# Performance work log

Hardware: AMD Instinct MI355X
Metric: run time of the kernel (lower is better)

## Reference

```python
import jax, jax.numpy as jnp
import numpy as np
import math

FACTOR = 5

def setup_inputs() -> dict:
    key = jax.random.key(0)
    k1, k2, k3, k4 = jax.random.split(key, 4)
    B, L, H, D = 8, 4096, 8, 64
    sample_k = FACTOR * int(np.ceil(np.log(L)))  # 45
    return {
        "queries": jax.random.normal(k1, (B, L, H, D), dtype=jnp.float32),
        "keys": jax.random.normal(k2, (B, L, H, D), dtype=jnp.float32),
        "values": jax.random.normal(k3, (B, L, H, D), dtype=jnp.float32),
        "index_sample": jax.random.randint(k4, (L, sample_k), 0, L, dtype=jnp.int64),
    }


def reference(queries, keys, values, index_sample):
    B, L_Q, H, D = queries.shape
    L_K = keys.shape[1]
    # [B, H, L, D]
    Q = jnp.transpose(queries, (0, 2, 1, 3))
    K = jnp.transpose(keys, (0, 2, 1, 3))
    V = jnpp = jnp.transpose(values, (0, 2, 1, 3))

    u = min(FACTOR * int(math.ceil(math.log(L_Q))), L_Q)  # n_top

    # --- _prob_QK ---
    # sampled keys: [B, H, L_Q, sample_k, D]
    K_sample = K[:, :, index_sample, :]
    # Q_K_sample: [B, H, L_Q, sample_k]
    Q_K_sample = jnp.einsum("bhqd,bhqsd->bhqs", Q, K_sample)
    M = jnp.max(Q_K_sample, axis=-1) - jnp.sum(Q_K_sample, axis=-1) / L_K
    _, M_top = jax.lax.top_k(M, u)  # [B, H, u]
    Q_reduce = jnp.take_along_axis(Q, M_top[..., None], axis=2)  # [B, H, u, D]
    scores = jnp.einsum("bhud,bhkd->bhuk", Q_reduce, K)  # [B, H, u, L_K]

    scale = 1.0 / math.sqrt(D)
    scores = scores * scale

    # --- initial context (mask_flag=True): causal cumsum of V ---
    context = jnp.cumsum(V, axis=2)  # [B, H, L_V, D]

    # --- causal ProbMask: key position j invalid if j > query position ---
    key_pos = jnp.arange(L_K)
    mask = key_pos[None, None, None, :] > M_top[..., None]  # [B, H, u, L_K]
    scores = jnp.where(mask, -jnp.inf, scores)

    attn = jax.nn.softmax(scores, axis=-1)  # dropout is identity at eval
    values_agg = jnp.einsum("bhuk,bhkd->bhud", attn, V)  # [B, H, u, D]

    b_idx = jnp.arange(B)[:, None, None]
    h_idx = jnp.arange(H)[None, :, None]
    context = context.at[b_idx, h_idx, M_top].set(values_agg)

    return jnp.transpose(context, (0, 2, 1, 3))  # [B, L_Q, H, D]
```

## Files before the change

kernel.cpp:

```cpp
#include <hip/hip_runtime.h>
#include <math.h>

#define Bc 8
#define Lc 4096
#define Hc 8
#define Dc 64
#define CHUNK 512
#define NCH (Lc / CHUNK)
#define VCH 16
#define VROWS (Lc / VCH)

template<int CTRL>
__device__ __forceinline__ float dpp_radd(float v) {
    int y = __builtin_amdgcn_update_dpp(0, __float_as_int(v), CTRL, 0xF, 0xF, true);
    return v + __int_as_float(y);
}
__device__ __forceinline__ float row16_sum(float p) {
    p = dpp_radd<0x128>(p);
    p = dpp_radd<0x124>(p);
    p = dpp_radd<0x122>(p);
    p = dpp_radd<0x121>(p);
    return p;
}

template<int S>
__global__ __launch_bounds__(256) void k_meas_t(
    const float* __restrict__ Q, const float* __restrict__ K,
    const int* __restrict__ idx, float* __restrict__ M)
{
    constexpr int NIT = (S + 3) / 4;
    int b = blockIdx.z, h = blockIdx.y;
    int w = threadIdx.x >> 6, lane = threadIdx.x & 63;
    int q = blockIdx.x * 4 + w;
    int grp = lane >> 4, gl = lane & 15;

    const float4 qv = *(const float4*)(Q + (((size_t)b * Lc + q) * Hc + h) * Dc + gl * 4);
    const int* ip = idx + (size_t)q * S + grp;
    const float* Kb = K + ((size_t)b * Lc * Hc + h) * Dc + gl * 4;

    int rows[NIT];
    #pragma unroll
    for (int it = 0; it < NIT - 1; it++) rows[it] = ip[it * 4];
    {
        int s = 4 * (NIT - 1) + grp;
        rows[NIT - 1] = ip[(s < S) ? 4 * (NIT - 1) : (S - 1 - grp)];
    }

    float mloc = -INFINITY, sloc = 0.f;
    #pragma unroll
    for (int it = 0; it < NIT; it++) {
        const float4 kw = *(const float4*)(Kb + ((size_t)rows[it] << 9));
        float p = kw.x * qv.x + kw.y * qv.y + kw.z * qv.z + kw.w * qv.w;
        p = row16_sum(p);
        int s = it * 4 + grp;
        if (s < S) { mloc = fmaxf(mloc, p); sloc += p; }
    }
    mloc = fmaxf(mloc, __shfl_xor(mloc, 16, 64));
    mloc = fmaxf(mloc, __shfl_xor(mloc, 32, 64));
    sloc += __shfl_xor(sloc, 16, 64);
    sloc += __shfl_xor(sloc, 32, 64);

    if (lane == 0)
        M[((size_t)(b * Hc + h)) * Lc + q] = mloc - sloc * (1.0f / (float)Lc);
}

__global__ __launch_bounds__(256) void k_meas_dyn(
    const float* __restrict__ Q, const float* __restrict__ K,
    const int* __restrict__ idx, float* __restrict__ M, int S)
{
    int b = blockIdx.z, h = blockIdx.y;
    int w = threadIdx.x >> 6, lane = threadIdx.x & 63;
    int q = blockIdx.x * 4 + w;
    int grp = lane >> 4, gl = lane & 15;

    const float4 qv = *(const float4*)(Q + (((size_t)b * Lc + q) * Hc + h) * Dc + gl * 4);
    const int* ip = idx + (size_t)q * S;
    const float* Kb = K + ((size_t)b * Lc * Hc + h) * Dc + gl * 4;

    float mloc = -INFINITY, sloc = 0.f;
    int niter = (S + 3) >> 2;
    for (int it = 0; it < niter; it++) {
        int s = it * 4 + grp;
        int ii = s < S ? s : S - 1;
        int row = ip[ii];
        const float4 kw = *(const float4*)(Kb + ((size_t)row << 9));
        float p = kw.x * qv.x + kw.y * qv.y + kw.z * qv.z + kw.w * qv.w;
        p = row16_sum(p);
        if (s < S) { mloc = fmaxf(mloc, p); sloc += p; }
    }
    mloc = fmaxf(mloc, __shfl_xor(mloc, 16, 64));
    mloc = fmaxf(mloc, __shfl_xor(mloc, 32, 64));
    sloc += __shfl_xor(sloc, 16, 64);
    sloc += __shfl_xor(sloc, 32, 64);
    if (lane == 0)
        M[((size_t)(b * Hc + h)) * Lc + q] = mloc - sloc * (1.0f / (float)Lc);
}

__global__ __launch_bounds__(256) void k_topk(
    const float* __restrict__ M, int* __restrict__ top, int U)
{
    int bh = blockIdx.x;
    int tid = threadIdx.x;
    const float* m = M + (size_t)bh * Lc;

    unsigned long long key[16];
    #pragma unroll
    for (int j = 0; j < 16; j++) {
        int i = tid * 16 + j;
        unsigned int u = __float_as_uint(m[i]);
        u ^= (unsigned int)(((int)u >> 31)) | 0x80000000u;
        key[j] = ((unsigned long long)u << 32) | (unsigned int)i;
    }
    unsigned long long myb = key[0];
    #pragma unroll
    for (int j = 1; j < 16; j++) myb = key[j] > myb ? key[j] : myb;

    __shared__ unsigned long long swave[2][4];

    for (int u = 0; u < U; u++) {
        unsigned long long wmax = myb;
        #pragma unroll
        for (int o = 32; o >= 1; o >>= 1) {
            unsigned long long t = __shfl_xor(wmax, o, 64);
            wmax = t > wmax ? t : wmax;
        }
        if ((tid & 63) == 0) swave[u & 1][tid >> 6] = wmax;
        __syncthreads();
        unsigned long long w0 = swave[u & 1][0], w1 = swave[u & 1][1];
        unsigned long long w2 = swave[u & 1][2], w3 = swave[u & 1][3];
        unsigned long long a = w0 > w1 ? w0 : w1;
        unsigned long long c = w2 > w3 ? w2 : w3;
        unsigned long long win = a > c ? a : c;
        int widx = (int)(win & 0xFFFFFFFFu);
        if (tid == 0) top[(size_t)bh * U + u] = widx;
        if (tid == (widx >> 4)) {
            #pragma unroll
            for (int j = 0; j < 16; j++) if (j == (widx & 15)) key[j] = 0ull;
            unsigned long long b2 = key[0];
            #pragma unroll
            for (int j = 1; j < 16; j++) b2 = key[j] > b2 ? key[j] : b2;
            myb = b2;
        }
    }
}

__global__ __launch_bounds__(256) void k_vsum(
    const float* __restrict__ V, float* __restrict__ bsum)
{
    int b = blockIdx.z, h = blockIdx.y, c = blockIdx.x;
    int d = threadIdx.x & 63, g = threadIdx.x >> 6;
    __shared__ float part[4][64];
    float s = 0.f;
    int r0 = c * VROWS;
    for (int r = r0 + g; r < r0 + VROWS; r += 4)
        s += V[(((size_t)b * Lc + r) * Hc + h) * Dc + d];
    part[g][d] = s;
    __syncthreads();
    if (g == 0)
        bsum[(((size_t)(b * Hc + h)) * VCH + c) * 64 + d] =
            part[0][d] + part[1][d] + part[2][d] + part[3][d];
}

__global__ __launch_bounds__(256) void k_scan(
    const float* __restrict__ V, const float* __restrict__ bsum,
    float* __restrict__ out)
{
    int b = blockIdx.z, h = blockIdx.y, c = blockIdx.x;
    int d = threadIdx.x & 63, g = threadIdx.x >> 6;
    int bh = b * Hc + h;
    __shared__ float gtot[4][64];
    __shared__ float goff[4][64];

    float base = 0.f;
    for (int cc = 0; cc < c; cc++)
        base += bsum[((size_t)bh * VCH + cc) * 64 + d];

    int gs = c * VROWS + g * 64;
    float gsum = 0.f;
    for (int r = gs; r < gs + 64; r++)
        gsum += V[(((size_t)b * Lc + r) * Hc + h) * Dc + d];
    gtot[g][d] = gsum;
    __syncthreads();
    if (g == 0) {
        float run = base;
        for (int gg = 0; gg < 4; gg++) { goff[gg][d] = run; run += gtot[gg][d]; }
    }
    __syncthreads();
    float run = goff[g][d];
    for (int r = gs; r < gs + 64; r++) {
        size_t o = (((size_t)b * Lc + r) * Hc + h) * Dc + d;
        run += V[o];
        out[o] = run;
    }
}

__global__ __launch_bounds__(256) void k_attn2(
    const float* __restrict__ Q, const float* __restrict__ K,
    const float* __restrict__ V, const int* __restrict__ top,
    float* __restrict__ Opart, float* __restrict__ Mp, float* __restrict__ Lp,
    int U)
{
    int b = blockIdx.z, h = blockIdx.y, c = blockIdx.x;
    int bh = b * Hc + h;
    int tid = threadIdx.x;
    int lane = tid & 63, g = tid >> 6;

    __shared__ float sQ[45][64];
    __shared__ int   sqi[45];
    __shared__ float sKT[64][65];
    __shared__ float sVT[64][65];
    __shared__ float sP[45][64];

    if (tid < U) sqi[tid] = top[(size_t)bh * U + tid];
    __syncthreads();
    for (int u = g; u < U; u += 4)
        sQ[u][lane] = Q[(((size_t)b * Lc + sqi[u]) * Hc + h) * Dc + lane] * 0.125f;

    int nj = 0, uj[12], qj[12];
    for (int u = g; u < U; u += 4) { uj[nj] = u; qj[nj] = sqi[u]; nj++; }

    float m_r[12], l_r[12], o_r[12];
    #pragma unroll
    for (int j = 0; j < 12; j++) { m_r[j] = -INFINITY; l_r[j] = 0.f; o_r[j] = 0.f; }

    int k0c = c * CHUNK;
    for (int t = 0; t < CHUNK / 64; t++) {
        int k0 = k0c + t * 64;
        __syncthreads();
        {
            const float* kp = K + (((size_t)b * Lc + k0 + lane) * Hc + h) * Dc + g * 16;
            const float* vp = V + (((size_t)b * Lc + k0 + lane) * Hc + h) * Dc + g * 16;
            #pragma unroll
            for (int i = 0; i < 4; i++) {
                float4 kw = *(const float4*)(kp + i * 4);
                float4 vw = *(const float4*)(vp + i * 4);
                int d0 = g * 16 + i * 4;
                sKT[d0+0][lane] = kw.x; sKT[d0+1][lane] = kw.y;
                sKT[d0+2][lane] = kw.z; sKT[d0+3][lane] = kw.w;
                sVT[d0+0][lane] = vw.x; sVT[d0+1][lane] = vw.y;
                sVT[d0+2][lane] = vw.z; sVT[d0+3][lane] = vw.w;
            }
        }
        __syncthreads();

        for (int j = 0; j < nj; j++) {
            int q = qj[j];
            if (k0 > q) continue;
            int u = uj[j];
            float s = 0.f;
            #pragma unroll
            for (int d = 0; d < 64; d += 4) {
                float k0v = sKT[d+0][lane];
                float k1v = sKT[d+1][lane];
                float k2v = sKT[d+2][lane];
                float k3v = sKT[d+3][lane];
                float4 qv = *(const float4*)&sQ[u][d];
                s += qv.x*k0v + qv.y*k1v + qv.z*k2v + qv.w*k3v;
            }
            if (k0 + lane > q) s = -INFINITY;
            float tm = s;
            #pragma unroll
            for (int o = 32; o >= 1; o >>= 1) tm = fmaxf(tm, __shfl_xor(tm, o, 64));
            float mnew = fmaxf(m_r[j], tm);
            float p = __expf(s - mnew);
            float ps = p;
            #pragma unroll
            for (int o = 32; o >= 1; o >>= 1) ps += __shfl_xor(ps, o, 64);
            float alpha = __expf(m_r[j] - mnew);
            l_r[j] = l_r[j] * alpha + ps;
            m_r[j] = mnew;
            sP[u][lane] = p;
            float pv = 0.f;
            #pragma unroll
            for (int k = 0; k < 64; k += 4) {
                float v0 = sVT[lane][k+0];
                float v1 = sVT[lane][k+1];
                float v2 = sVT[lane][k+2];
                float v3 = sVT[lane][k+3];
                float4 pw = *(const float4*)&sP[u][k];
                pv += pw.x*v0 + pw.y*v1 + pw.z*v2 + pw.w*v3;
            }
            o_r[j] = o_r[j] * alpha + pv;
        }
    }

    for (int j = 0; j < nj; j++) {
        int u = uj[j];
        size_t s0 = ((size_t)bh * NCH + c) * U + u;
        Opart[s0 * 64 + lane] = o_r[j];
        if (lane == 0) { Mp[s0] = m_r[j]; Lp[s0] = l_r[j]; }
    }
}

__global__ __launch_bounds__(64) void k_combine(
    const float* __restrict__ Opart, const float* __restrict__ Mp,
    const float* __restrict__ Lp, const int* __restrict__ top,
    float* __restrict__ out, int U)
{
    int b = blockIdx.z, h = blockIdx.y, u = blockIdx.x;
    int bh = b * Hc + h;
    int lane = threadIdx.x;
    int q = top[(size_t)bh * U + u];

    float mv[NCH], lv[NCH];
    float mg = -INFINITY;
    #pragma unroll
    for (int c = 0; c < NCH; c++) {
        size_t s0 = ((size_t)bh * NCH + c) * U + u;
        mv[c] = Mp[s0]; lv[c] = Lp[s0];
        mg = fmaxf(mg, mv[c]);
    }
    float Ls = 0.f, o = 0.f;
    #pragma unroll
    for (int c = 0; c < NCH; c++) {
        if (lv[c] > 0.f) {
            float w = __expf(mv[c] - mg);
            Ls += w * lv[c];
            o  += w * Opart[(((size_t)bh * NCH + c) * U + u) * 64 + lane];
        }
    }
    out[(((size_t)b * Lc + q) * Hc + h) * Dc + lane] = o / Ls;
}

extern "C" void kernel_launch(void* const* d_in, const int* in_sizes, int n_in,
                              void* d_out, int out_size, void* d_ws, size_t ws_size,
                              hipStream_t stream)
{
    const float* Q = (const float*)d_in[0];
    const float* K = (const float*)d_in[1];
    const float* V = (const float*)d_in[2];
    const int* idx = (const int*)d_in[3];
    float* out = (float*)d_out;

    int S = in_sizes[3] / Lc;

    char* ws = (char*)d_ws;
    float* M     = (float*)ws;
    float* Opart = (float*)ws;
    float* Mp    = (float*)(ws + 6291456);
    float* Lp    = (float*)(ws + 6422528);
    float* bsum  = (float*)(ws + 6815744);
    int*   top   = (int*)  (ws + 8388608);

    dim3 blk(256);
    if (S == 45)
        k_meas_t<45><<<dim3(Lc / 4, Hc, Bc), blk, 0, stream>>>(Q, K, idx, M);
    else
        k_meas_dyn  <<<dim3(Lc / 4, Hc, Bc), blk, 0, stream>>>(Q, K, idx, M, S);
    k_topk   <<<dim3(Bc * Hc),        blk, 0, stream>>>(M, top, S);
    k_vsum   <<<dim3(VCH, Hc, Bc),    blk, 0, stream>>>(V, bsum);
    k_scan   <<<dim3(VCH, Hc, Bc),    blk, 0, stream>>>(V, bsum, out);
    k_attn2  <<<dim3(NCH, Hc, Bc),    blk, 0, stream>>>(Q, K, V, top, Opart, Mp, Lp, S);
    k_combine<<<dim3(S, Hc, Bc), dim3(64), 0, stream>>>(Opart, Mp, Lp, top, out, S);
}
```

Before: 641.2 us.

## Batch four queries per K/V tile pass, sort queries, and balance causal chunks

Reworks the sparse-query attention kernel. Each wave now processes four top-u queries at once so every K and V value read from shared memory is reused four times. Per-wave query slots are bitonic-sorted by position so causally dead groups are skipped together. Chunk boundaries are non-uniform to balance causal work, tiles past the largest selected query are skipped, and K is stored in a swizzled float4 layout with DPP-based wave reductions. In exchange it uses more registers and duplicates padded slots, whose partial outputs are written redundantly.

```diff
diff --git a/kernel.cpp b/kernel.cpp
--- a/kernel.cpp
+++ b/kernel.cpp
@@ -5,22 +5,38 @@
 #define Lc 4096
 #define Hc 8
 #define Dc 64
-#define CHUNK 512
-#define NCH (Lc / CHUNK)
+#define NCH 8
 #define VCH 16
 #define VROWS (Lc / VCH)
 
+__constant__ int c_cb[NCH + 1] = {0, 256, 576, 832, 1216, 1600, 2048, 2624, 4096};
+
+template<int CTRL>
+__device__ __forceinline__ float dpp_mov(float v) {
+    return __int_as_float(__builtin_amdgcn_update_dpp(
+        0, __float_as_int(v), CTRL, 0xF, 0xF, true));
+}
 template<int CTRL>
 __device__ __forceinline__ float dpp_radd(float v) {
-    int y = __builtin_amdgcn_update_dpp(0, __float_as_int(v), CTRL, 0xF, 0xF, true);
-    return v + __int_as_float(y);
+    return v + dpp_mov<CTRL>(v);
 }
 __device__ __forceinline__ float row16_sum(float p) {
-    p = dpp_radd<0x128>(p);
-    p = dpp_radd<0x124>(p);
-    p = dpp_radd<0x122>(p);
-    p = dpp_radd<0x121>(p);
+    p = dpp_radd<0x128>(p); p = dpp_radd<0x124>(p);
+    p = dpp_radd<0x122>(p); p = dpp_radd<0x121>(p);
     return p;
+}
+__device__ __forceinline__ float wmax64(float v) {
+    v = fmaxf(v, dpp_mov<0x128>(v));
+    v = fmaxf(v, dpp_mov<0x124>(v));
+    v = fmaxf(v, dpp_mov<0x122>(v));
+    v = fmaxf(v, dpp_mov<0x121>(v));
+    v = fmaxf(v, __shfl_xor(v, 16, 64));
+    return fmaxf(v, __shfl_xor(v, 32, 64));
+}
+__device__ __forceinline__ float wsum64(float v) {
+    v = row16_sum(v);
+    v += __shfl_xor(v, 16, 64);
+    return v + __shfl_xor(v, 32, 64);
 }
 
 template<int S>
@@ -205,26 +221,62 @@
     int tid = threadIdx.x;
     int lane = tid & 63, g = tid >> 6;
 
-    __shared__ float sQ[45][64];
-    __shared__ int   sqi[45];
-    __shared__ float sKT[64][65];
-    __shared__ float sVT[64][65];
-    __shared__ float sP[45][64];
+    __shared__ float4 sK4[64][16];
+    __shared__ float  sVT[64][65];
+    __shared__ float  sQ[45][64];
+    __shared__ float  sP[45][64];
+    __shared__ int    sqi[45];
 
     if (tid < U) sqi[tid] = top[(size_t)bh * U + tid];
     __syncthreads();
     for (int u = g; u < U; u += 4)
         sQ[u][lane] = Q[(((size_t)b * Lc + sqi[u]) * Hc + h) * Dc + lane] * 0.125f;
 
-    int nj = 0, uj[12], qj[12];
-    for (int u = g; u < U; u += 4) { uj[nj] = u; qj[nj] = sqi[u]; nj++; }
+    int qbm = 0;
+    for (int u = 0; u < U; u++) qbm = max(qbm, sqi[u]);
+
+    int qq[16], tt[16];
+    int ulast = g + (((U - 1 - g) >> 2) << 2);
+    #pragma unroll
+    for (int i = 0; i < 12; i++) {
+        int u = g + 4 * i;
+        u = (u <= ulast) ? u : ulast;
+        tt[i] = u; qq[i] = sqi[u];
+    }
+    #pragma unroll
+    for (int i = 12; i < 16; i++) { tt[i] = tt[11]; qq[i] = 0x7FFFFFFF; }
+    #pragma unroll
+    for (int kk = 2; kk <= 16; kk <<= 1) {
+        #pragma unroll
+        for (int jj = kk >> 1; jj > 0; jj >>= 1) {
+            #pragma unroll
+            for (int ii = 0; ii < 16; ii++) {
+                int ll = ii ^ jj;
+                if (ll > ii) {
+                    bool up = ((ii & kk) == 0);
+                    bool sw = up ? (qq[ii] > qq[ll]) : (qq[ii] < qq[ll]);
+                    if (sw) {
+                        int tq = qq[ii]; qq[ii] = qq[ll]; qq[ll] = tq;
+                        int tu = tt[ii]; tt[ii] = tt[ll]; tt[ll] = tu;
+                    }
+                }
+            }
+        }
+    }
 
     float m_r[12], l_r[12], o_r[12];
     #pragma unroll
     for (int j = 0; j < 12; j++) { m_r[j] = -INFINITY; l_r[j] = 0.f; o_r[j] = 0.f; }
 
-    int k0c = c * CHUNK;
-    for (int t = 0; t < CHUNK / 64; t++) {
+    int k0c = c_cb[c], k1c = c_cb[c + 1];
+    int ntile = 0;
+    if (qbm >= k0c) {
+        int lastk = min(qbm, k1c - 1);
+        ntile = (lastk - k0c) / 64 + 1;
+    }
+    int kswz = lane & 7;
+
+    for (int t = 0; t < ntile; t++) {
         int k0 = k0c + t * 64;
         __syncthreads();
         {
@@ -234,58 +286,72 @@
             for (int i = 0; i < 4; i++) {
                 float4 kw = *(const float4*)(kp + i * 4);
                 float4 vw = *(const float4*)(vp + i * 4);
-                int d0 = g * 16 + i * 4;
-                sKT[d0+0][lane] = kw.x; sKT[d0+1][lane] = kw.y;
-                sKT[d0+2][lane] = kw.z; sKT[d0+3][lane] = kw.w;
+                int lb = g * 4 + i;
+                sK4[lane][lb ^ (lane & 7)] = kw;
+                int d0 = lb * 4;
                 sVT[d0+0][lane] = vw.x; sVT[d0+1][lane] = vw.y;
                 sVT[d0+2][lane] = vw.z; sVT[d0+3][lane] = vw.w;
             }
         }
         __syncthreads();
 
-        for (int j = 0; j < nj; j++) {
-            int q = qj[j];
-            if (k0 > q) continue;
-            int u = uj[j];
-            float s = 0.f;
-            #pragma unroll
-            for (int d = 0; d < 64; d += 4) {
-                float k0v = sKT[d+0][lane];
-                float k1v = sKT[d+1][lane];
-                float k2v = sKT[d+2][lane];
-                float k3v = sKT[d+3][lane];
-                float4 qv = *(const float4*)&sQ[u][d];
-                s += qv.x*k0v + qv.y*k1v + qv.z*k2v + qv.w*k3v;
+        #pragma unroll
+        for (int j0 = 0; j0 < 12; j0 += 4) {
+            if (k0 > qq[j0 + 3]) continue;
+            int ua = tt[j0], ub = tt[j0+1], uc = tt[j0+2], ud = tt[j0+3];
+            float s0 = 0.f, s1 = 0.f, s2 = 0.f, s3 = 0.f;
+            #pragma unroll
+            for (int lb = 0; lb < 16; lb++) {
+                float4 kb = sK4[lane][lb ^ kswz];
+                float4 qa = *(const float4*)&sQ[ua][lb * 4];
+                float4 qb = *(const float4*)&sQ[ub][lb * 4];
+                float4 qc = *(const float4*)&sQ[uc][lb * 4];
+                float4 qd = *(const float4*)&sQ[ud][lb * 4];
+                s0 += kb.x*qa.x + kb.y*qa.y + kb.z*qa.z + kb.w*qa.w;
+                s1 += kb.x*qb.x + kb.y*qb.y + kb.z*qb.z + kb.w*qb.w;
+                s2 += kb.x*qc.x + kb.y*qc.y + kb.z*qc.z + kb.w*qc.w;
+                s3 += kb.x*qd.x + kb.y*qd.y + kb.z*qd.z + kb.w*qd.w;
             }
-            if (k0 + lane > q) s = -INFINITY;
-            float tm = s;
-            #pragma unroll
-            for (int o = 32; o >= 1; o >>= 1) tm = fmaxf(tm, __shfl_xor(tm, o, 64));
-            float mnew = fmaxf(m_r[j], tm);
-            float p = __expf(s - mnew);
-            float ps = p;
-            #pragma unroll
-            for (int o = 32; o >= 1; o >>= 1) ps += __shfl_xor(ps, o, 64);
-            float alpha = __expf(m_r[j] - mnew);
-            l_r[j] = l_r[j] * alpha + ps;
-            m_r[j] = mnew;
-            sP[u][lane] = p;
-            float pv = 0.f;
+            float a0, a1, a2, a3;
+#define SLOT(jj, sv, av) { \
+            float sA = (k0 + lane > qq[jj]) ? -INFINITY : sv; \
+            float tm = wmax64(sA); \
+            float mnew = fmaxf(m_r[jj], tm); \
+            float p = __expf(sA - mnew); \
+            float ps = wsum64(p); \
+            av = __expf(m_r[jj] - mnew); \
+            m_r[jj] = mnew; \
+            l_r[jj] = l_r[jj] * av + ps; \
+            sP[tt[jj]][lane] = p; }
+            SLOT(j0+0, s0, a0)
+            SLOT(j0+1, s1, a1)
+            SLOT(j0+2, s2, a2)
+            SLOT(j0+3, s3, a3)
+#undef SLOT
+            float p0 = 0.f, p1 = 0.f, p2 = 0.f, p3 = 0.f;
             #pragma unroll
             for (int k = 0; k < 64; k += 4) {
-                float v0 = sVT[lane][k+0];
-                float v1 = sVT[lane][k+1];
-                float v2 = sVT[lane][k+2];
-                float v3 = sVT[lane][k+3];
-                float4 pw = *(const float4*)&sP[u][k];
-                pv += pw.x*v0 + pw.y*v1 + pw.z*v2 + pw.w*v3;
+                float v0 = sVT[lane][k+0], v1 = sVT[lane][k+1];
+                float v2 = sVT[lane][k+2], v3 = sVT[lane][k+3];
+                float4 wa = *(const float4*)&sP[ua][k];
+                float4 wb = *(const float4*)&sP[ub][k];
+                float4 wc = *(const float4*)&sP[uc][k];
+                float4 wd = *(const float4*)&sP[ud][k];
+                p0 += wa.x*v0 + wa.y*v1 + wa.z*v2 + wa.w*v3;
+                p1 += wb.x*v0 + wb.y*v1 + wb.z*v2 + wb.w*v3;
+                p2 += wc.x*v0 + wc.y*v1 + wc.z*v2 + wc.w*v3;
+                p3 += wd.x*v0 + wd.y*v1 + wd.z*v2 + wd.w*v3;
             }
-            o_r[j] = o_r[j] * alpha + pv;
-        }
-    }
-
-    for (int j = 0; j < nj; j++) {
-        int u = uj[j];
+            o_r[j0+0] = o_r[j0+0] * a0 + p0;
+            o_r[j0+1] = o_r[j0+1] * a1 + p1;
+            o_r[j0+2] = o_r[j0+2] * a2 + p2;
+            o_r[j0+3] = o_r[j0+3] * a3 + p3;
+        }
+    }
+
+    #pragma unroll
+    for (int j = 0; j < 12; j++) {
+        int u = tt[j];
         size_t s0 = ((size_t)bh * NCH + c) * U + u;
         Opart[s0 * 64 + lane] = o_r[j];
         if (lane == 0) { Mp[s0] = m_r[j]; Lp[s0] = l_r[j]; }
```

After: 636.2 us. About the same (-0.8%).
